# Kernel tuning notes

Measured on AMD Instinct MI355X. Metric: run time of the kernel, lower is better.

## Reference

```python
import jax, jax.numpy as jnp
import numpy as np

B, S, H = 2, 1024, 2048
F_DIM = 1408        # per-expert ffn dim
SF_DIM = 5632       # shared expert ffn dim
E = 8               # num_experts
TOP_K = 2
NORM_TOPK_PROB = False


def setup_inputs() -> dict:
    key = jax.random.key(0)
    ks = jax.random.split(key, 9)
    w = lambda k, shp: (jax.random.normal(k, shp, dtype=jnp.float32) * 0.02)
    return {
        "hidden_states": jax.random.normal(ks[0], (B, S, H), dtype=jnp.float32),
        "gate_w": w(ks[1], (E, H)),                 # router Linear(H -> E), no bias
        "gate_proj_w": w(ks[2], (E, F_DIM, H)),     # stacked expert gate_proj weights
        "up_proj_w": w(ks[3], (E, F_DIM, H)),
        "down_proj_w": w(ks[4], (E, H, F_DIM)),
        "shared_gate_proj_w": w(ks[5], (SF_DIM, H)),
        "shared_up_proj_w": w(ks[6], (SF_DIM, H)),
        "shared_down_proj_w": w(ks[7], (H, SF_DIM)),
        "shared_expert_gate_w": w(ks[8], (1, H)),   # Linear(H -> 1), no bias
    }


def reference(hidden_states, gate_w, gate_proj_w, up_proj_w, down_proj_w,
              shared_gate_proj_w, shared_up_proj_w, shared_down_proj_w,
              shared_expert_gate_w):
    b, s, h = hidden_states.shape
    x = hidden_states.reshape(-1, h)                              # [T, H]
    # router: softmax in fp32 -> top_k
    logits = x @ gate_w.T                                         # [T, E]
    probs = jax.nn.softmax(logits.astype(jnp.float32), axis=-1)
    rw, sel = jax.lax.top_k(probs, TOP_K)                         # [T, K]
    if NORM_TOPK_PROB:
        rw = rw / jnp.sum(rw, axis=-1, keepdims=True)
    rw = rw.astype(x.dtype)
    # dense one-hot dispatch weights [T, E]
    wm = jnp.sum(jax.nn.one_hot(sel, E, dtype=rw.dtype) * rw[..., None], axis=1)
    # all experts on all tokens (dense dispatch, as in the original)
    g = jax.nn.silu(jnp.einsum('th,efh->tef', x, gate_proj_w))    # [T, E, F]
    u = jnp.einsum('th,efh->tef', x, up_proj_w)
    routed = jnp.einsum('tef,ehf,te->th', g * u, down_proj_w, wm) # [T, H]
    # shared expert with scalar sigmoid gate
    sg = jax.nn.silu(x @ shared_gate_proj_w.T) * (x @ shared_up_proj_w.T)
    shared = sg @ shared_down_proj_w.T                            # [T, H]
    gate_val = jax.nn.sigmoid(x @ shared_expert_gate_w.T)         # [T, 1]
    out = routed + gate_val * shared
    return out.reshape(b, s, h)
```

## Files before the change

kernel.cpp:

```cpp
#include <hip/hip_runtime.h>

#define TT 2048
#define HD 2048
#define FD 1408
#define SFD 5632
#define NE 8
#define BM 128
#define BN 128
#define BK 32

using f32x4 = __attribute__((ext_vector_type(4))) float;
using s16x8 = __attribute__((ext_vector_type(8))) short;
typedef unsigned short us;

__device__ __forceinline__ us f2bf(float f) {
    union { float f; unsigned u; } v; v.f = f;
    unsigned r = v.u + 0x7fff + ((v.u >> 16) & 1);
    return (us)(r >> 16);
}
__device__ __forceinline__ float bf2f(us u) {
    union { unsigned u; float f; } v; v.u = ((unsigned)u) << 16;
    return v.f;
}
__device__ __forceinline__ unsigned cvt2(float a, float b) {
    union { float f; unsigned u; } va, vb; va.f = a; vb.f = b;
    unsigned ra = va.u + 0x8000u, rb = vb.u + 0x8000u;
    return (rb & 0xffff0000u) | (ra >> 16);
}
__device__ __forceinline__ s16x8 pack8(f32x4 h0, f32x4 h1) {
    union { unsigned u[4]; s16x8 s; } r;
    r.u[0] = cvt2(h0[0], h0[1]); r.u[1] = cvt2(h0[2], h0[3]);
    r.u[2] = cvt2(h1[0], h1[1]); r.u[3] = cvt2(h1[2], h1[3]);
    return r.s;
}

__device__ __forceinline__ void gload16(const void* g, void* l) {
    __builtin_amdgcn_global_load_lds(
        (const __attribute__((address_space(1))) unsigned*)g,
        (__attribute__((address_space(3))) unsigned*)l, 16, 0, 0);
}

__device__ __forceinline__ void cvt_tile(const float* __restrict__ src,
                                         us* __restrict__ dst, int blk) {
    size_t i = ((size_t)blk * 256 + threadIdx.x) * 8;
    float4 f0 = *(const float4*)(src + i);
    float4 f1 = *(const float4*)(src + i + 4);
    s16x8 v;
    v[0]=(short)f2bf(f0.x); v[1]=(short)f2bf(f0.y); v[2]=(short)f2bf(f0.z); v[3]=(short)f2bf(f0.w);
    v[4]=(short)f2bf(f1.x); v[5]=(short)f2bf(f1.y); v[6]=(short)f2bf(f1.z); v[7]=(short)f2bf(f1.w);
    *(s16x8*)(dst + i) = v;
}

__global__ void cvt_kernel(const float* __restrict__ x, us* __restrict__ xb) {
    cvt_tile(x, xb, blockIdx.x);
}

__global__ void router_cvt_kernel(const float* __restrict__ x, const float* __restrict__ gw,
                                  const float* __restrict__ segw,
                                  int* counts, int* tlist, float* wlist, float* gateval,
                                  int* selpos,
                                  const float* __restrict__ gpw, const float* __restrict__ upw,
                                  const float* __restrict__ sgw, const float* __restrict__ suw,
                                  us* gpw_b, us* upw_b, us* sgw_b, us* suw_b, us* xb) {
    int hw = blockIdx.x;
    if (hw >= 512) {
        int i = hw - 512;
        if      (i < 11264) cvt_tile(gpw, gpw_b, i);
        else if (i < 22528) cvt_tile(upw, upw_b, i - 11264);
        else if (i < 28160) cvt_tile(sgw, sgw_b, i - 22528);
        else if (i < 33792) cvt_tile(suw, suw_b, i - 28160);
        else                cvt_tile(x,   xb,    i - 33792);
        return;
    }
    int wave = threadIdx.x >> 6;
    int lane = threadIdx.x & 63;
    int t = hw * 4 + wave;
    float acc[9];
    #pragma unroll
    for (int i = 0; i < 9; ++i) acc[i] = 0.f;
    const float* xrow = x + (size_t)t * HD;
    for (int h = lane; h < HD; h += 64) {
        float xv = xrow[h];
        #pragma unroll
        for (int e = 0; e < NE; ++e) acc[e] += xv * gw[e * HD + h];
        acc[8] += xv * segw[h];
    }
    #pragma unroll
    for (int i = 0; i < 9; ++i) {
        float v = acc[i];
        #pragma unroll
        for (int s = 32; s > 0; s >>= 1) v += __shfl_xor(v, s);
        acc[i] = v;
    }
    if (lane == 0) {
        float m = acc[0];
        #pragma unroll
        for (int e = 1; e < NE; ++e) m = fmaxf(m, acc[e]);
        float p[NE], sum = 0.f;
        #pragma unroll
        for (int e = 0; e < NE; ++e) { p[e] = expf(acc[e] - m); sum += p[e]; }
        float inv = 1.f / sum;
        int b1 = 0, b2 = -1; float v1 = p[0], v2 = -1.f;
        #pragma unroll
        for (int e = 1; e < NE; ++e) {
            if (p[e] > v1) { v2 = v1; b2 = b1; v1 = p[e]; b1 = e; }
            else if (p[e] > v2) { v2 = p[e]; b2 = e; }
        }
        v1 *= inv; v2 *= inv;
        int s1 = atomicAdd(&counts[b1], 1); tlist[b1 * TT + s1] = t; wlist[b1 * TT + s1] = v1;
        int s2 = atomicAdd(&counts[b2], 1); tlist[b2 * TT + s2] = t; wlist[b2 * TT + s2] = v2;
        selpos[2 * t]     = b1 * TT + s1;
        selpos[2 * t + 1] = b2 * TT + s2;
        gateval[t] = 1.f / (1.f + expf(-acc[8]));
    }
}

__global__ void router_kernel(const float* __restrict__ x, const float* __restrict__ gw,
                              const float* __restrict__ segw,
                              int* counts, int* tlist, float* wlist, float* gateval,
                              int* selpos) {
    int wave = threadIdx.x >> 6;
    int lane = threadIdx.x & 63;
    int t = blockIdx.x * 4 + wave;
    float acc[9];
    #pragma unroll
    for (int i = 0; i < 9; ++i) acc[i] = 0.f;
    const float* xrow = x + (size_t)t * HD;
    for (int h = lane; h < HD; h += 64) {
        float xv = xrow[h];
        #pragma unroll
        for (int e = 0; e < NE; ++e) acc[e] += xv * gw[e * HD + h];
        acc[8] += xv * segw[h];
    }
    #pragma unroll
    for (int i = 0; i < 9; ++i) {
        float v = acc[i];
        #pragma unroll
        for (int s = 32; s > 0; s >>= 1) v += __shfl_xor(v, s);
        acc[i] = v;
    }
    if (lane == 0) {
        float m = acc[0];
        #pragma unroll
        for (int e = 1; e < NE; ++e) m = fmaxf(m, acc[e]);
        float p[NE], sum = 0.f;
        #pragma unroll
        for (int e = 0; e < NE; ++e) { p[e] = expf(acc[e] - m); sum += p[e]; }
        float inv = 1.f / sum;
        int b1 = 0, b2 = -1; float v1 = p[0], v2 = -1.f;
        #pragma unroll
        for (int e = 1; e < NE; ++e) {
            if (p[e] > v1) { v2 = v1; b2 = b1; v1 = p[e]; b1 = e; }
            else if (p[e] > v2) { v2 = p[e]; b2 = e; }
        }
        v1 *= inv; v2 *= inv;
        int s1 = atomicAdd(&counts[b1], 1); tlist[b1 * TT + s1] = t; wlist[b1 * TT + s1] = v1;
        int s2 = atomicAdd(&counts[b2], 1); tlist[b2 * TT + s2] = t; wlist[b2 * TT + s2] = v2;
        selpos[2 * t]     = b1 * TT + s1;
        selpos[2 * t + 1] = b2 * TT + s2;
        gateval[t] = 1.f / (1.f + expf(-acc[8]));
    }
}

__global__ void prefix_kernel(const int* counts, int* offsets) {
    if (threadIdx.x == 0) {
        int s = 0;
        for (int e = 0; e < NE; ++e) { offsets[e] = s; s += counts[e]; }
    }
}

__global__ void combine_full(const int* __restrict__ selpos, const float* __restrict__ wlist,
                             const int* __restrict__ offsets, const float* __restrict__ gateval,
                             const float* __restrict__ sdpart, const us* __restrict__ robuf,
                             float* __restrict__ out) {
    int t = blockIdx.x;
    int p0 = selpos[2 * t], p1 = selpos[2 * t + 1];
    float w0 = wlist[p0], w1 = wlist[p1];
    int r0 = offsets[p0 >> 11] + (p0 & (TT - 1));
    int r1 = offsets[p1 >> 11] + (p1 & (TT - 1));
    float g = gateval[t];
    int c = threadIdx.x * 8;
    const float* s0 = sdpart + (size_t)t * HD + c;
    const float* s1 = sdpart + (size_t)TT * HD + (size_t)t * HD + c;
    s16x8 a = *(const s16x8*)(robuf + (size_t)r0 * HD + c);
    s16x8 b = *(const s16x8*)(robuf + (size_t)r1 * HD + c);
    float* op = out + (size_t)t * HD + c;
    #pragma unroll
    for (int j = 0; j < 8; ++j)
        op[j] = g * (s0[j] + s1[j]) + w0 * bf2f((us)a[j]) + w1 * bf2f((us)b[j]);
}

__global__ void combine_add(const int* __restrict__ selpos, const float* __restrict__ wlist,
                            const int* __restrict__ offsets,
                            const us* __restrict__ robuf, float* __restrict__ out) {
    int t = blockIdx.x;
    int p0 = selpos[2 * t], p1 = selpos[2 * t + 1];
    float w0 = wlist[p0], w1 = wlist[p1];
    int r0 = offsets[p0 >> 11] + (p0 & (TT - 1));
    int r1 = offsets[p1 >> 11] + (p1 & (TT - 1));
    int c = threadIdx.x * 8;
    s16x8 a = *(const s16x8*)(robuf + (size_t)r0 * HD + c);
    s16x8 b = *(const s16x8*)(robuf + (size_t)r1 * HD + c);
    float* op = out + (size_t)t * HD + c;
    #pragma unroll
    for (int j = 0; j < 8; ++j)
        op[j] += w0 * bf2f((us)a[j]) + w1 * bf2f((us)b[j]);
}

#define GU_TOT   2112
#define GU_CHUNK (GU_TOT / 8)
#define DN_TOT   1280
#define DN_CHUNK (DN_TOT / 8)
#define GU_CVT   16896

__global__ __launch_bounds__(256, 3)
void gemm6(const us* __restrict__ xb,
           const us* __restrict__ Bg_s, const us* __restrict__ Bu_s,
           const us* __restrict__ Bg_r, const us* __restrict__ Bu_r,
           us* __restrict__ Cs, us* __restrict__ Cr,
           const int* __restrict__ counts, const int* __restrict__ offsets,
           const int* __restrict__ tlist,
           const float* __restrict__ sdw_f, const float* __restrict__ dpw_f,
           us* sdw_b, us* dpw_b) {
    __shared__ s16x8 Asl[2][512];
    __shared__ s16x8 B0l[2][512];
    __shared__ s16x8 B1l[2][512];

    int hw = blockIdx.x;
    if (hw >= GU_TOT) {
        int i = hw - GU_TOT;
        if (i < 5632) cvt_tile(sdw_f, sdw_b, i);
        else          cvt_tile(dpw_f, dpw_b, i - 5632);
        return;
    }
    int flat = (hw & 7) * GU_CHUNK + (hw >> 3);
    int pi = flat >> 4, mt = flat & 15;
    int grpIdx = pi / 3, pos = pi % 3;
    int z, nt;
    if (pos == 0) { z = 0; nt = grpIdx; }
    else { int ri = grpIdx * 2 + (pos - 1); z = 1 + ri / 11; nt = ri % 11; }

    bool sp = (z == 0);
    int e = z - 1;
    int M = sp ? TT : counts[e];
    int n0 = nt * BN;
    int m0 = mt * BM;
    if (M == 0 || m0 >= M) return;
    int row_off = sp ? 0 : offsets[e];
    const us* B0p = sp ? Bg_s : Bg_r + (size_t)e * FD * HD;
    const us* B1p = sp ? Bu_s : Bu_r + (size_t)e * FD * HD;

    int tid = threadIdx.x;
    int lane = tid & 63, w = tid >> 6;

    const us* aptr[2];
    const us* b0ptr[2];
    const us* b1ptr[2];
    #pragma unroll
    for (int j = 0; j < 2; ++j) {
        int r = 32 * w + 16 * j + (lane >> 2);
        int c = (lane & 3) ^ ((r >> 1) & 3);
        int ar = m0 + r; if (ar > M - 1) ar = M - 1;
        size_t arow = sp ? (size_t)ar : (size_t)tlist[e * TT + ar];
        aptr[j]  = xb + arow * HD + c * 8;
        b0ptr[j] = B0p + (size_t)(n0 + r) * HD + c * 8;
        b1ptr[j] = B1p + (size_t)(n0 + r) * HD + c * 8;
    }

    int wm = (w >> 1) * 64, wn = (w & 1) * 64;
    int grp = lane >> 4, l16 = lane & 15;

    f32x4 acc0[4][4], acc1[4][4];
    f32x4 zero = {0.f, 0.f, 0.f, 0.f};
    #pragma unroll
    for (int mi = 0; mi < 4; ++mi)
        #pragma unroll
        for (int ni = 0; ni < 4; ++ni) { acc0[mi][ni] = zero; acc1[mi][ni] = zero; }

    auto stage = [&](int buf, int k0) {
        #pragma unroll
        for (int j = 0; j < 2; ++j)
            gload16(aptr[j] + k0, (void*)&Asl[buf][(32 * w + 16 * j) * 4]);
        #pragma unroll
        for (int j = 0; j < 2; ++j)
            gload16(b0ptr[j] + k0, (void*)&B0l[buf][(32 * w + 16 * j) * 4]);
        #pragma unroll
        for (int j = 0; j < 2; ++j)
            gload16(b1ptr[j] + k0, (void*)&B1l[buf][(32 * w + 16 * j) * 4]);
    };

    stage(0, 0);
    int cur = 0;
    const int NT = HD / BK;
    for (int kt = 0; kt < NT; ++kt) {
        __syncthreads();
        if (kt + 1 < NT) stage(cur ^ 1, (kt + 1) * BK);
        s16x8 af[4];
        #pragma unroll
        for (int mi = 0; mi < 4; ++mi) {
            int rr = wm + mi * 16 + l16;
            af[mi] = Asl[cur][rr * 4 + (grp ^ ((rr >> 1) & 3))];
        }
        #pragma unroll
        for (int ni = 0; ni < 4; ++ni) {
            int rb = wn + ni * 16 + l16;
            int slot = rb * 4 + (grp ^ ((rb >> 1) & 3));
            s16x8 b0 = B0l[cur][slot];
            #pragma unroll
            for (int mi = 0; mi < 4; ++mi)
                acc0[mi][ni] = __builtin_amdgcn_mfma_f32_16x16x32_bf16(af[mi], b0, acc0[mi][ni], 0, 0, 0);
            s16x8 b1 = B1l[cur][slot];
            #pragma unroll
            for (int mi = 0; mi < 4; ++mi)
                acc1[mi][ni] = __builtin_amdgcn_mfma_f32_16x16x32_bf16(af[mi], b1, acc1[mi][ni], 0, 0, 0);
        }
        cur ^= 1;
    }

    #pragma unroll
    for (int mi = 0; mi < 4; ++mi) {
        #pragma unroll
        for (int r_ = 0; r_ < 4; ++r_) {
            int mrow = m0 + wm + mi * 16 + (lane >> 4) * 4 + r_;
            if (mrow >= M) continue;
            #pragma unroll
            for (int ni = 0; ni < 4; ++ni) {
                int col = n0 + wn + ni * 16 + l16;
                float g = acc0[mi][ni][r_], u = acc1[mi][ni][r_];
                float val = g * u / (1.f + __expf(-g));
                if (sp) Cs[(size_t)mrow * SFD + col] = f2bf(val);
                else    Cr[(size_t)(row_off + mrow) * FD + col] = f2bf(val);
            }
        }
    }
}

__global__ __launch_bounds__(256, 3)
void gemm_down(const us* __restrict__ Ashared, const us* __restrict__ Arouted,
               const us* __restrict__ Bshared, const us* __restrict__ Brouted,
               float* __restrict__ Cshared, us* __restrict__ Crouted,
               const int* __restrict__ counts, const int* __restrict__ offsets) {
    __shared__ s16x8 Asl[2][512];
    __shared__ s16x8 Bsl[2][1024];

    int hw = blockIdx.x;
    int flat = (hw & 7) * DN_CHUNK + (hw >> 3);
    int pi = flat >> 4, mt = flat & 15;
    int grpIdx = pi / 5, pos = pi % 5;
    int z, nt;
    if (pos == 0) { z = grpIdx >> 3; nt = grpIdx & 7; }
    else { int ri = grpIdx * 4 + (pos - 1); z = 2 + (ri >> 3); nt = ri & 7; }

    bool sp = (z < 2);
    int e = z - 2;
    int M = sp ? TT : counts[e];
    int n0 = nt * 256;
    int m0 = mt * BM;
    if (M == 0 || m0 >= M) return;
    int row_off = sp ? 0 : offsets[e];
    int NT = sp ? (SFD / 2 / BK) : (FD / BK);
    int lda = sp ? SFD : FD;
    int kofs = sp ? z * (SFD / 2) : 0;
    const us* Abase = (sp ? Ashared : Arouted) + kofs;
    const us* Bbase = (sp ? Bshared : Brouted + (size_t)e * HD * FD) + kofs;

    int tid = threadIdx.x;
    int lane = tid & 63, w = tid >> 6;

    const us* aptr[2];
    #pragma unroll
    for (int j = 0; j < 2; ++j) {
        int r = 32 * w + 16 * j + (lane >> 2);
        int c = (lane & 3) ^ ((r >> 1) & 3);
        int ar = m0 + r; if (ar > M - 1) ar = M - 1;
        size_t arow = sp ? (size_t)ar : (size_t)(row_off + ar);
        aptr[j] = Abase + arow * lda + c * 8;
    }
    const us* bptr[4];
    #pragma unroll
    for (int j = 0; j < 4; ++j) {
        int r = 64 * w + 16 * j + (lane >> 2);
        int c = (lane & 3) ^ ((r >> 1) & 3);
        bptr[j] = Bbase + (size_t)(n0 + r) * lda + c * 8;
    }

    int wm = (w >> 1) * 64, wn = (w & 1) * 128;
    int grp = lane >> 4, l16 = lane & 15;

    f32x4 acc[4][8];
    f32x4 zero = {0.f, 0.f, 0.f, 0.f};
    #pragma unroll
    for (int mi = 0; mi < 4; ++mi)
        #pragma unroll
        for (int ni = 0; ni < 8; ++ni) acc[mi][ni] = zero;

    auto stage = [&](int buf, int k0) {
        #pragma unroll
        for (int j = 0; j < 2; ++j)
            gload16(aptr[j] + k0, (void*)&Asl[buf][(32 * w + 16 * j) * 4]);
        #pragma unroll
        for (int j = 0; j < 4; ++j)
            gload16(bptr[j] + k0, (void*)&Bsl[buf][(64 * w + 16 * j) * 4]);
    };

    stage(0, 0);
    int cur = 0;
    for (int kt = 0; kt < NT; ++kt) {
        __syncthreads();
        if (kt + 1 < NT) stage(cur ^ 1, (kt + 1) * BK);
        s16x8 af[4];
        #pragma unroll
        for (int mi = 0; mi < 4; ++mi) {
            int rr = wm + mi * 16 + l16;
            af[mi] = Asl[cur][rr * 4 + (grp ^ ((rr >> 1) & 3))];
        }
        #pragma unroll
        for (int ni = 0; ni < 8; ++ni) {
            int rb = wn + ni * 16 + l16;
            s16x8 bf = Bsl[cur][rb * 4 + (grp ^ ((rb >> 1) & 3))];
            #pragma unroll
            for (int mi = 0; mi < 4; ++mi)
                acc[mi][ni] = __builtin_amdgcn_mfma_f32_16x16x32_bf16(af[mi], bf, acc[mi][ni], 0, 0, 0);
        }
        cur ^= 1;
    }

    #pragma unroll
    for (int mi = 0; mi < 4; ++mi) {
        #pragma unroll
        for (int r_ = 0; r_ < 4; ++r_) {
            int mrow = m0 + wm + mi * 16 + (lane >> 4) * 4 + r_;
            if (mrow >= M) continue;
            #pragma unroll
            for (int ni = 0; ni < 8; ++ni) {
                int col = n0 + wn + ni * 16 + l16;
                float v = acc[mi][ni][r_];
                if (sp) Cshared[(size_t)z * TT * HD + (size_t)mrow * HD + col] = v;
                else    Crouted[(size_t)(row_off + mrow) * HD + col] = f2bf(v);
            }
        }
    }
}

template<int EPI, bool GATHER>
__global__ __launch_bounds__(256, 2)
void gemm4(const us* __restrict__ A, int lda,
           const float* __restrict__ B, size_t eStrideB, int ldb, int K,
           int Mfixed, const int* __restrict__ counts, const int* __restrict__ offsets,
           const int* __restrict__ tlist, const float* __restrict__ wlist,
           us* __restrict__ C, int ldc,
           const float* __restrict__ gateval, float* __restrict__ out, int ldout) {
    __shared__ s16x8 As[3][512];
    __shared__ f32x4 Bs[3][1024];

    int e = blockIdx.z;
    int M = counts ? counts[e] : Mfixed;
    int n0 = blockIdx.x * BN;
    int m0 = blockIdx.y * BM;
    if (M == 0 || m0 >= M) return;
    int row_off = offsets ? offsets[e] : 0;
    const float* Bp = B + (size_t)e * eStrideB;

    int tid = threadIdx.x;
    int lane = tid & 63, w = tid >> 6;

    const us* aptr[2];
    #pragma unroll
    for (int j = 0; j < 2; ++j) {
        int r = 32 * w + 16 * j + (lane >> 2);
        int c = (lane & 3) ^ (r & 3);
        int ar = m0 + r; if (ar > M - 1) ar = M - 1;
        size_t grow;
        if constexpr (GATHER) grow = (size_t)tlist[e * TT + ar];
        else                  grow = (size_t)(row_off + ar);
        aptr[j] = A + grow * (size_t)lda + c * 8;
    }
    const float* bptr[4];
    #pragma unroll
    for (int j = 0; j < 4; ++j) {
        int r = 32 * w + 8 * j + (lane >> 3);
        int c = (lane & 7) ^ (r & 7);
        bptr[j] = Bp + (size_t)(n0 + r) * ldb + c * 4;
    }

    int wm = (w >> 1) * 64, wn = (w & 1) * 64;
    int grp = lane >> 4, l16 = lane & 15;

    f32x4 acc[4][4];
    f32x4 zero = {0.f, 0.f, 0.f, 0.f};
    #pragma unroll
    for (int mi = 0; mi < 4; ++mi)
        #pragma unroll
        for (int ni = 0; ni < 4; ++ni) acc[mi][ni] = zero;

    auto stage = [&](int buf, int k0) {
        #pragma unroll
        for (int j = 0; j < 2; ++j)
            gload16(aptr[j] + k0, (void*)&As[buf][(32 * w + 16 * j) * 4]);
        #pragma unroll
        for (int j = 0; j < 4; ++j)
            gload16(bptr[j] + k0, (void*)&Bs[buf][(32 * w + 8 * j) * 8]);
    };

    int NT = K / BK;
    stage(0, 0);
    stage(1, BK);
    for (int kt = 0; kt < NT; ++kt) {
        int cur = kt % 3;
        __builtin_amdgcn_s_barrier();
        if (kt + 2 < NT) {
            stage((kt + 2) % 3, (kt + 2) * BK);
            asm volatile("s_waitcnt vmcnt(12)" ::: "memory");
        } else if (kt + 1 < NT) {
            asm volatile("s_waitcnt vmcnt(6)" ::: "memory");
        } else {
            asm volatile("s_waitcnt vmcnt(0)" ::: "memory");
        }
        s16x8 af[4];
        #pragma unroll
        for (int mi = 0; mi < 4; ++mi) {
            int rr = wm + mi * 16 + l16;
            af[mi] = As[cur][rr * 4 + (grp ^ (rr & 3))];
        }
        #pragma unroll
        for (int ni = 0; ni < 4; ++ni) {
            int rb = wn + ni * 16 + l16;
            int s0 = (2 * grp) ^ (rb & 7);
            f32x4 h0 = Bs[cur][rb * 8 + s0];
            f32x4 h1 = Bs[cur][rb * 8 + (s0 ^ 1)];
            s16x8 bfr = pack8(h0, h1);
            #pragma unroll
            for (int mi = 0; mi < 4; ++mi)
                acc[mi][ni] = __builtin_amdgcn_mfma_f32_16x16x32_bf16(af[mi], bfr, acc[mi][ni], 0, 0, 0);
        }
    }

    #pragma unroll
    for (int mi = 0; mi < 4; ++mi) {
        #pragma unroll
        for (int r_ = 0; r_ < 4; ++r_) {
            int mrow = m0 + wm + mi * 16 + (lane >> 4) * 4 + r_;
            if (mrow >= M) continue;
            #pragma unroll
            for (int ni = 0; ni < 4; ++ni) {
                int col = n0 + wn + ni * 16 + l16;
                float v = acc[mi][ni][r_];
                if constexpr (EPI == 0) {
                    C[(size_t)(row_off + mrow) * ldc + col] = f2bf(v);
                } else if constexpr (EPI == 1) {
                    size_t idx = (size_t)(row_off + mrow) * ldc + col;
                    float g = bf2f(C[idx]);
                    C[idx] = f2bf(g * v / (1.f + __expf(-g)));
                } else if constexpr (EPI == 2) {
                    int tok = tlist[e * TT + mrow]; float wv = wlist[e * TT + mrow];
                    atomicAdd(out + (size_t)tok * ldout + col, wv * v);
                } else {
                    out[(size_t)mrow * ldout + col] = gateval[mrow] * v;
                }
            }
        }
    }
}

extern "C" void kernel_launch(void* const* d_in, const int* in_sizes, int n_in,
                              void* d_out, int out_size, void* d_ws, size_t ws_size,
                              hipStream_t stream) {
    const float* x    = (const float*)d_in[0];
    const float* gw   = (const float*)d_in[1];
    const float* gpw  = (const float*)d_in[2];
    const float* upw  = (const float*)d_in[3];
    const float* dpw  = (const float*)d_in[4];
    const float* sgw  = (const float*)d_in[5];
    const float* suw  = (const float*)d_in[6];
    const float* sdw  = (const float*)d_in[7];
    const float* segw = (const float*)d_in[8];
    float* out = (float*)d_out;
    char* ws = (char*)d_ws;

    int*   counts  = (int*)(ws + 0);
    int*   offsets = (int*)(ws + 64);
    int*   tlist   = (int*)(ws + 256);
    float* wlist   = (float*)(ws + 65792);
    float* gateval = (float*)(ws + 131328);
    int*   selpos  = (int*)(ws + 139520);

    hipMemsetAsync(counts, 0, 64, stream);

    size_t need_main = 301203456ull;
    if (ws_size >= need_main) {
        us* xb     = (us*)(ws + 262144);
        us* gpw_b  = (us*)(ws + 8650752);
        us* upw_b  = (us*)(ws + 54788096);
        us* dpw_b  = (us*)(ws + 100925440);
        us* sgw_b  = (us*)(ws + 147062784);
        us* suw_b  = (us*)(ws + 170131456);
        us* sdw_b  = (us*)(ws + 193200128);
        us* gbuf_s = (us*)(ws + 216268800);
        us* gbuf_r = (us*)(ws + 239337472);
        us* robuf  = (us*)(ws + 250871808);
        float* sdpart = (float*)(ws + 267649024);

        router_cvt_kernel<<<dim3(512 + 35840), 256, 0, stream>>>(
            x, gw, segw, counts, tlist, wlist, gateval, selpos,
            gpw, upw, sgw, suw, gpw_b, upw_b, sgw_b, suw_b, xb);
        prefix_kernel<<<dim3(1), 64, 0, stream>>>(counts, offsets);

        gemm6<<<dim3(GU_TOT + GU_CVT), 256, 0, stream>>>(
            xb, sgw_b, suw_b, gpw_b, upw_b, gbuf_s, gbuf_r, counts, offsets, tlist,
            sdw, dpw, sdw_b, dpw_b);
        gemm_down<<<dim3(DN_TOT), 256, 0, stream>>>(
            gbuf_s, gbuf_r, sdw_b, dpw_b, sdpart, robuf, counts, offsets);

        combine_full<<<dim3(TT), 256, 0, stream>>>(selpos, wlist, offsets, gateval, sdpart, robuf, out);
        return;
    }

    us* xb    = (us*)(ws + 155904);
    us* gbuf  = (us*)(ws + 8544512);
    us* robuf = (us*)(ws + 20078848);
    size_t need_fb = 20078848 + (size_t)4096 * HD * 2;

    router_kernel<<<dim3(TT / 4), 256, 0, stream>>>(x, gw, segw, counts, tlist, wlist, gateval, selpos);
    prefix_kernel<<<dim3(1), 64, 0, stream>>>(counts, offsets);
    cvt_kernel<<<dim3(TT * HD / 2048), 256, 0, stream>>>(x, xb);

    gemm4<0, false><<<dim3(SFD / BN, TT / BM, 1), 256, 0, stream>>>(
        xb, HD, sgw, 0, HD, HD, TT, nullptr, nullptr, nullptr, nullptr, gbuf, SFD, nullptr, nullptr, 0);
    gemm4<1, false><<<dim3(SFD / BN, TT / BM, 1), 256, 0, stream>>>(
        xb, HD, suw, 0, HD, HD, TT, nullptr, nullptr, nullptr, nullptr, gbuf, SFD, nullptr, nullptr, 0);
    gemm4<3, false><<<dim3(HD / BN, TT / BM, 1), 256, 0, stream>>>(
        gbuf, SFD, sdw, 0, SFD, SFD, TT, nullptr, nullptr, nullptr, nullptr, nullptr, 0, gateval, out, HD);

    gemm4<0, true><<<dim3(FD / BN, TT / BM, NE), 256, 0, stream>>>(
        xb, HD, gpw, (size_t)FD * HD, HD, HD, 0, counts, offsets, tlist, nullptr, gbuf, FD, nullptr, nullptr, 0);
    gemm4<1, true><<<dim3(FD / BN, TT / BM, NE), 256, 0, stream>>>(
        xb, HD, upw, (size_t)FD * HD, HD, HD, 0, counts, offsets, tlist, nullptr, gbuf, FD, nullptr, nullptr, 0);

    if (ws_size >= need_fb) {
        gemm4<0, false><<<dim3(HD / BN, TT / BM, NE), 256, 0, stream>>>(
            gbuf, FD, dpw, (size_t)HD * FD, FD, FD, 0, counts, offsets, nullptr, nullptr, robuf, HD, nullptr, nullptr, 0);
        combine_add<<<dim3(TT), 256, 0, stream>>>(selpos, wlist, offsets, robuf, out);
    } else {
        gemm4<2, false><<<dim3(HD / BN, TT / BM, NE), 256, 0, stream>>>(
            gbuf, FD, dpw, (size_t)HD * FD, FD, FD, 0, counts, offsets, tlist, wlist, nullptr, 0, nullptr, out, HD);
    }
}
```

Before: 453.6 us.

## Use 512-thread blocks with smaller per-wave tiles in gate/up and down GEMMs

Both main GEMM kernels move from 256 to 512 threads per block (8 waves) while keeping the 128x128 block tile, so each wave owns a smaller sub-tile and holds half as many accumulators. The staging loads are redistributed so each thread issues fewer global-to-LDS copies, and the fused weight-conversion blocks are resized to 512 threads (half as many blocks). The aim is to cut register pressure and raise occupancy and latency hiding. In exchange, each wave does fewer MFMAs per LDS fragment read, which lowers register-level reuse and adds LDS traffic per FLOP.

```diff
diff --git a/kernel.cpp b/kernel.cpp
--- a/kernel.cpp
+++ b/kernel.cpp
@@ -22,17 +22,6 @@
     union { unsigned u; float f; } v; v.u = ((unsigned)u) << 16;
     return v.f;
 }
-__device__ __forceinline__ unsigned cvt2(float a, float b) {
-    union { float f; unsigned u; } va, vb; va.f = a; vb.f = b;
-    unsigned ra = va.u + 0x8000u, rb = vb.u + 0x8000u;
-    return (rb & 0xffff0000u) | (ra >> 16);
-}
-__device__ __forceinline__ s16x8 pack8(f32x4 h0, f32x4 h1) {
-    union { unsigned u[4]; s16x8 s; } r;
-    r.u[0] = cvt2(h0[0], h0[1]); r.u[1] = cvt2(h0[2], h0[3]);
-    r.u[2] = cvt2(h1[0], h1[1]); r.u[3] = cvt2(h1[2], h1[3]);
-    return r.s;
-}
 
 __device__ __forceinline__ void gload16(const void* g, void* l) {
     __builtin_amdgcn_global_load_lds(
@@ -43,6 +32,16 @@
 __device__ __forceinline__ void cvt_tile(const float* __restrict__ src,
                                          us* __restrict__ dst, int blk) {
     size_t i = ((size_t)blk * 256 + threadIdx.x) * 8;
+    float4 f0 = *(const float4*)(src + i);
+    float4 f1 = *(const float4*)(src + i + 4);
+    s16x8 v;
+    v[0]=(short)f2bf(f0.x); v[1]=(short)f2bf(f0.y); v[2]=(short)f2bf(f0.z); v[3]=(short)f2bf(f0.w);
+    v[4]=(short)f2bf(f1.x); v[5]=(short)f2bf(f1.y); v[6]=(short)f2bf(f1.z); v[7]=(short)f2bf(f1.w);
+    *(s16x8*)(dst + i) = v;
+}
+__device__ __forceinline__ void cvt_tile512(const float* __restrict__ src,
+                                            us* __restrict__ dst, int blk) {
+    size_t i = ((size_t)blk * 512 + threadIdx.x) * 8;
     float4 f0 = *(const float4*)(src + i);
     float4 f1 = *(const float4*)(src + i + 4);
     s16x8 v;
@@ -211,9 +210,9 @@
 #define GU_CHUNK (GU_TOT / 8)
 #define DN_TOT   1280
 #define DN_CHUNK (DN_TOT / 8)
-#define GU_CVT   16896
-
-__global__ __launch_bounds__(256, 3)
+#define GU_CVT   8448
+
+__global__ __launch_bounds__(512, 4)
 void gemm6(const us* __restrict__ xb,
            const us* __restrict__ Bg_s, const us* __restrict__ Bu_s,
            const us* __restrict__ Bg_r, const us* __restrict__ Bu_r,
@@ -229,8 +228,8 @@
     int hw = blockIdx.x;
     if (hw >= GU_TOT) {
         int i = hw - GU_TOT;
-        if (i < 5632) cvt_tile(sdw_f, sdw_b, i);
-        else          cvt_tile(dpw_f, dpw_b, i - 5632);
+        if (i < 2816) cvt_tile512(sdw_f, sdw_b, i);
+        else          cvt_tile512(dpw_f, dpw_b, i - 2816);
         return;
     }
     int flat = (hw & 7) * GU_CHUNK + (hw >> 3);
@@ -253,40 +252,28 @@
     int tid = threadIdx.x;
     int lane = tid & 63, w = tid >> 6;
 
-    const us* aptr[2];
-    const us* b0ptr[2];
-    const us* b1ptr[2];
-    #pragma unroll
-    for (int j = 0; j < 2; ++j) {
-        int r = 32 * w + 16 * j + (lane >> 2);
-        int c = (lane & 3) ^ ((r >> 1) & 3);
-        int ar = m0 + r; if (ar > M - 1) ar = M - 1;
-        size_t arow = sp ? (size_t)ar : (size_t)tlist[e * TT + ar];
-        aptr[j]  = xb + arow * HD + c * 8;
-        b0ptr[j] = B0p + (size_t)(n0 + r) * HD + c * 8;
-        b1ptr[j] = B1p + (size_t)(n0 + r) * HD + c * 8;
-    }
-
-    int wm = (w >> 1) * 64, wn = (w & 1) * 64;
+    int sr = tid >> 2;
+    int sc = (lane & 3) ^ ((sr >> 1) & 3);
+    int ar = m0 + sr; if (ar > M - 1) ar = M - 1;
+    size_t arow = sp ? (size_t)ar : (size_t)tlist[e * TT + ar];
+    const us* aptr  = xb  + arow * HD + sc * 8;
+    const us* b0ptr = B0p + (size_t)(n0 + sr) * HD + sc * 8;
+    const us* b1ptr = B1p + (size_t)(n0 + sr) * HD + sc * 8;
+
+    int wm = (w >> 2) * 64, wn = (w & 3) * 32;
     int grp = lane >> 4, l16 = lane & 15;
 
-    f32x4 acc0[4][4], acc1[4][4];
+    f32x4 acc0[4][2], acc1[4][2];
     f32x4 zero = {0.f, 0.f, 0.f, 0.f};
     #pragma unroll
     for (int mi = 0; mi < 4; ++mi)
         #pragma unroll
-        for (int ni = 0; ni < 4; ++ni) { acc0[mi][ni] = zero; acc1[mi][ni] = zero; }
+        for (int ni = 0; ni < 2; ++ni) { acc0[mi][ni] = zero; acc1[mi][ni] = zero; }
 
     auto stage = [&](int buf, int k0) {
-        #pragma unroll
-        for (int j = 0; j < 2; ++j)
-            gload16(aptr[j] + k0, (void*)&Asl[buf][(32 * w + 16 * j) * 4]);
-        #pragma unroll
-        for (int j = 0; j < 2; ++j)
-            gload16(b0ptr[j] + k0, (void*)&B0l[buf][(32 * w + 16 * j) * 4]);
-        #pragma unroll
-        for (int j = 0; j < 2; ++j)
-            gload16(b1ptr[j] + k0, (void*)&B1l[buf][(32 * w + 16 * j) * 4]);
+        gload16(aptr  + k0, (void*)&Asl[buf][16 * w * 4]);
+        gload16(b0ptr + k0, (void*)&B0l[buf][16 * w * 4]);
+        gload16(b1ptr + k0, (void*)&B1l[buf][16 * w * 4]);
     };
 
     stage(0, 0);
@@ -302,7 +289,7 @@
             af[mi] = Asl[cur][rr * 4 + (grp ^ ((rr >> 1) & 3))];
         }
         #pragma unroll
-        for (int ni = 0; ni < 4; ++ni) {
+        for (int ni = 0; ni < 2; ++ni) {
             int rb = wn + ni * 16 + l16;
             int slot = rb * 4 + (grp ^ ((rb >> 1) & 3));
             s16x8 b0 = B0l[cur][slot];
@@ -324,7 +311,7 @@
             int mrow = m0 + wm + mi * 16 + (lane >> 4) * 4 + r_;
             if (mrow >= M) continue;
             #pragma unroll
-            for (int ni = 0; ni < 4; ++ni) {
+            for (int ni = 0; ni < 2; ++ni) {
                 int col = n0 + wn + ni * 16 + l16;
                 float g = acc0[mi][ni][r_], u = acc1[mi][ni][r_];
                 float val = g * u / (1.f + __expf(-g));
@@ -335,7 +322,7 @@
     }
 }
 
-__global__ __launch_bounds__(256, 3)
+__global__ __launch_bounds__(512, 4)
 void gemm_down(const us* __restrict__ Ashared, const us* __restrict__ Arouted,
                const us* __restrict__ Bshared, const us* __restrict__ Brouted,
                float* __restrict__ Cshared, us* __restrict__ Crouted,
@@ -367,40 +354,34 @@
     int tid = threadIdx.x;
     int lane = tid & 63, w = tid >> 6;
 
-    const us* aptr[2];
+    int sr = tid >> 2;
+    int sc = (lane & 3) ^ ((sr >> 1) & 3);
+    int ar = m0 + sr; if (ar > M - 1) ar = M - 1;
+    size_t arow = sp ? (size_t)ar : (size_t)(row_off + ar);
+    const us* aptr = Abase + arow * lda + sc * 8;
+    const us* bptr[2];
     #pragma unroll
     for (int j = 0; j < 2; ++j) {
         int r = 32 * w + 16 * j + (lane >> 2);
         int c = (lane & 3) ^ ((r >> 1) & 3);
-        int ar = m0 + r; if (ar > M - 1) ar = M - 1;
-        size_t arow = sp ? (size_t)ar : (size_t)(row_off + ar);
-        aptr[j] = Abase + arow * lda + c * 8;
-    }
-    const us* bptr[4];
-    #pragma unroll
-    for (int j = 0; j < 4; ++j) {
-        int r = 64 * w + 16 * j + (lane >> 2);
-        int c = (lane & 3) ^ ((r >> 1) & 3);
         bptr[j] = Bbase + (size_t)(n0 + r) * lda + c * 8;
     }
 
-    int wm = (w >> 1) * 64, wn = (w & 1) * 128;
+    int wm = (w >> 2) * 64, wn = (w & 3) * 64;
     int grp = lane >> 4, l16 = lane & 15;
 
-    f32x4 acc[4][8];
+    f32x4 acc[4][4];
     f32x4 zero = {0.f, 0.f, 0.f, 0.f};
     #pragma unroll
     for (int mi = 0; mi < 4; ++mi)
         #pragma unroll
-        for (int ni = 0; ni < 8; ++ni) acc[mi][ni] = zero;
+        for (int ni = 0; ni < 4; ++ni) acc[mi][ni] = zero;
 
     auto stage = [&](int buf, int k0) {
+        gload16(aptr + k0, (void*)&Asl[buf][16 * w * 4]);
         #pragma unroll
         for (int j = 0; j < 2; ++j)
-            gload16(aptr[j] + k0, (void*)&Asl[buf][(32 * w + 16 * j) * 4]);
-        #pragma unroll
-        for (int j = 0; j < 4; ++j)
-            gload16(bptr[j] + k0, (void*)&Bsl[buf][(64 * w + 16 * j) * 4]);
+            gload16(bptr[j] + k0, (void*)&Bsl[buf][(32 * w + 16 * j) * 4]);
     };
 
     stage(0, 0);
@@ -415,7 +396,7 @@
             af[mi] = Asl[cur][rr * 4 + (grp ^ ((rr >> 1) & 3))];
         }
         #pragma unroll
-        for (int ni = 0; ni < 8; ++ni) {
+        for (int ni = 0; ni < 4; ++ni) {
             int rb = wn + ni * 16 + l16;
             s16x8 bf = Bsl[cur][rb * 4 + (grp ^ ((rb >> 1) & 3))];
             #pragma unroll
@@ -432,7 +413,7 @@
             int mrow = m0 + wm + mi * 16 + (lane >> 4) * 4 + r_;
             if (mrow >= M) continue;
             #pragma unroll
-            for (int ni = 0; ni < 8; ++ni) {
+            for (int ni = 0; ni < 4; ++ni) {
                 int col = n0 + wn + ni * 16 + l16;
                 float v = acc[mi][ni][r_];
                 if (sp) Cshared[(size_t)z * TT * HD + (size_t)mrow * HD + col] = v;
@@ -440,6 +421,18 @@
             }
         }
     }
+}
+
+__device__ __forceinline__ unsigned cvt2(float a, float b) {
+    union { float f; unsigned u; } va, vb; va.f = a; vb.f = b;
+    unsigned ra = va.u + 0x8000u, rb = vb.u + 0x8000u;
+    return (rb & 0xffff0000u) | (ra >> 16);
+}
+__device__ __forceinline__ s16x8 pack8(f32x4 h0, f32x4 h1) {
+    union { unsigned u[4]; s16x8 s; } r;
+    r.u[0] = cvt2(h0[0], h0[1]); r.u[1] = cvt2(h0[2], h0[3]);
+    r.u[2] = cvt2(h1[0], h1[1]); r.u[3] = cvt2(h1[2], h1[3]);
+    return r.s;
 }
 
 template<int EPI, bool GATHER>
@@ -605,10 +598,10 @@
             gpw, upw, sgw, suw, gpw_b, upw_b, sgw_b, suw_b, xb);
         prefix_kernel<<<dim3(1), 64, 0, stream>>>(counts, offsets);
 
-        gemm6<<<dim3(GU_TOT + GU_CVT), 256, 0, stream>>>(
+        gemm6<<<dim3(GU_TOT + GU_CVT), 512, 0, stream>>>(
             xb, sgw_b, suw_b, gpw_b, upw_b, gbuf_s, gbuf_r, counts, offsets, tlist,
             sdw, dpw, sdw_b, dpw_b);
-        gemm_down<<<dim3(DN_TOT), 256, 0, stream>>>(
+        gemm_down<<<dim3(DN_TOT), 512, 0, stream>>>(
             gbuf_s, gbuf_r, sdw_b, dpw_b, sdpart, robuf, counts, offsets);
 
         combine_full<<<dim3(TT), 256, 0, stream>>>(selpos, wlist, offsets, gateval, sdpart, robuf, out);
```

Result: faster. 442.9 us (-2.4%).
